# Kernel optimization log

Hardware: AMD Instinct MI355X
Metric: run time of the kernel (lower is better)

Reference implementation:

```python
import jax, jax.numpy as jnp
import numpy as np

NEG = -1e20

def _rope(x):
    # x: (N, L, H, D). Original buffers use inv_freq over D with D/2 entries;
    # sin/cos tiled to full D to broadcast (original code's einsum was under-specified for 4D).
    L, D = x.shape[1], x.shape[3]
    inv_freq = 1.0 / (10000.0 ** (jnp.arange(0, D, 2, dtype=jnp.float32) / D))
    t = jnp.arange(L, dtype=jnp.float32)
    freqs = t[:, None] * inv_freq[None, :]            # (L, D/2)
    sin = jnp.concatenate([jnp.sin(freqs)] * 2, -1)[None, :, None, :]  # (1,L,1,D)
    cos = jnp.concatenate([jnp.cos(freqs)] * 2, -1)[None, :, None, :]
    return x * cos + jnp.flip(x, -1) * sin

def setup_inputs() -> dict:
    key = jax.random.key(0)
    ks = jax.random.split(key, 8)
    N, L, E, H = 2, 1024, 2048, 16
    D = E // H
    s = 0.02
    return {
        "values": jax.random.normal(ks[0], (N, L, E), jnp.float32),
        "keys": jax.random.normal(ks[1], (N, L, E), jnp.float32),
        "queries": jax.random.normal(ks[2], (N, L, E), jnp.float32),
        "mask": jax.random.randint(ks[3], (N, 1, L, L), 0, 2, jnp.int32),
        "Wv": jax.random.normal(ks[4], (D, D), jnp.float32) * s,
        "Wk": jax.random.normal(ks[5], (D, D), jnp.float32) * s,
        "Wq": jax.random.normal(ks[6], (D, D), jnp.float32) * s,
        "Wo": jax.random.normal(ks[7], (E, E), jnp.float32) * s,
        "bo": jnp.zeros((E,), jnp.float32),
    }

def reference(values, keys, queries, mask, Wv, Wk, Wq, Wo, bo):
    N, L, E = queries.shape
    H = 16
    D = E // H
    v = values.reshape(N, L, H, D)
    k = keys.reshape(N, L, H, D)
    q = queries.reshape(N, L, H, D)
    q = _rope(q)
    k = _rope(k)
    # per-head linears (nn.Linear: x @ W.T)
    v = jnp.einsum('nlhd,od->nlho', v, Wv)
    k = jnp.einsum('nlhd,od->nlho', k, Wk)
    q = jnp.einsum('nlhd,od->nlho', q, Wq)
    energy = jnp.einsum('nqhd,nkhd->nhqk', q, k)
    energy = jnp.where(mask == 0, NEG, energy)
    attn = jax.nn.softmax(energy / jnp.sqrt(jnp.float32(E)), axis=3)
    out = jnp.einsum('nhqk,nkhd->nqhd', attn, v).reshape(N, L, E)
    return out @ Wo.T + bo
```

## Files before the change

### kernel.cpp

```cpp
#include <hip/hip_runtime.h>

#define LQ 1024
#define EMB 2048
#define NH 16
#define HD 128
#define RSCALE 0.022097086912079608f

typedef unsigned short u16x8 __attribute__((ext_vector_type(8)));
typedef __bf16 bf16x8 __attribute__((ext_vector_type(8)));
typedef float f32x4 __attribute__((ext_vector_type(4)));
typedef short s16x4 __attribute__((ext_vector_type(4)));

typedef const __attribute__((address_space(1))) unsigned int* gas_t;
typedef __attribute__((address_space(3))) unsigned int* las_t;

__device__ __forceinline__ void glds16(const void* g, void* l){
  __builtin_amdgcn_global_load_lds((gas_t)g, (las_t)l, 16, 0, 0);
}
__device__ __forceinline__ unsigned short f2b(float f){
  unsigned int x = __float_as_uint(f);
  return (unsigned short)((x + 0x7fffu + ((x >> 16) & 1u)) >> 16);
}
__device__ __forceinline__ short f2bs(float f){
  union { __bf16 h; short s; } c; c.h = (__bf16)f; return c.s;
}
__device__ __forceinline__ bf16x8 as_bf(u16x8 u){
  union { u16x8 u; bf16x8 b; } c; c.u = u; return c.b;
}
__device__ __forceinline__ f32x4 mfma16(s16x4 a, s16x4 b, f32x4 c){
  return __builtin_amdgcn_mfma_f32_16x16x16bf16_1k(a, b, c, 0, 0, 0);
}

__global__ __launch_bounds__(256) void k_prep(const float* __restrict__ Wo,
                                              unsigned short* __restrict__ Wob,
                                              const int* __restrict__ M,
                                              unsigned long long* __restrict__ Mb){
  int bx = blockIdx.x, t = threadIdx.x;
  if (bx < 4096) {
    int i = (bx * 256 + t) * 4;
    float4 f = *(const float4*)&Wo[i];
    ushort4 u;
    u.x = f2b(f.x); u.y = f2b(f.y); u.z = f2b(f.z); u.w = f2b(f.w);
    *(ushort4*)&Wob[i] = u;
  } else {
    int w_idx = (bx - 4096) * 4 + (t >> 6);
    int lane = t & 63;
    int n = w_idx >> 14, row = (w_idx >> 4) & 1023, wc = w_idx & 15;
    int v = M[(size_t)n * (LQ * LQ) + (size_t)row * LQ + wc * 64 + lane];
    unsigned long long b = __ballot(v != 0);
    if (lane == 0) Mb[w_idx] = b;
  }
}

__global__ __launch_bounds__(256) void k_proj(
    const float* __restrict__ vals, const float* __restrict__ keys,
    const float* __restrict__ qrys,
    const float* __restrict__ Wv, const float* __restrict__ Wk,
    const float* __restrict__ Wq,
    unsigned short* __restrict__ vp, unsigned short* __restrict__ kp,
    unsigned short* __restrict__ qp)
{
  __shared__ unsigned short Xs[64 * 136];
  __shared__ unsigned short Ws[128 * 136];
  __shared__ float scC[4 * 128], scS[4 * 128];
  int t = threadIdx.x;
  int which = blockIdx.y;
  const float* X; const float* W; unsigned short* OUT; bool rope;
  if (which == 0)      { X = vals; W = Wv; OUT = vp; rope = false; }
  else if (which == 1) { X = keys; W = Wk; OUT = kp; rope = true;  }
  else                 { X = qrys; W = Wq; OUT = qp; rope = true;  }
  float qs = (which == 2) ? RSCALE : 1.0f;
  int m0 = blockIdx.x * 64;

  #pragma unroll
  for (int i = 0; i < 8; ++i) {
    int ci = t + 256 * i;
    int row = ci >> 4, ch = ci & 15;
    float4 a = *(const float4*)&W[row * 128 + ch * 8];
    float4 b = *(const float4*)&W[row * 128 + ch * 8 + 4];
    u16x8 u;
    u[0]=f2b(a.x); u[1]=f2b(a.y); u[2]=f2b(a.z); u[3]=f2b(a.w);
    u[4]=f2b(b.x); u[5]=f2b(b.y); u[6]=f2b(b.z); u[7]=f2b(b.w);
    *(u16x8*)&Ws[row * 136 + ch * 8] = u;
  }
  if (rope) {
    int l0 = (blockIdx.x * 4) & 1023;
    #pragma unroll
    for (int i = 0; i < 2; ++i) {
      int idx = t + 256 * i;
      int li = idx >> 7, d = idx & 127, j = d & 63;
      float inv = 1.0f / powf(10000.0f, (float)(2 * j) * 0.0078125f);
      float ang = (float)(l0 + li) * inv;
      scC[idx] = cosf(ang);
      scS[idx] = sinf(ang);
    }
  }
  __syncthreads();
  #pragma unroll
  for (int i = 0; i < 8; ++i) {
    int fi = t + 256 * i;
    int row = fi >> 5, dq = (fi & 31) * 4;
    int gr = m0 + row;
    float4 x = *(const float4*)&X[(size_t)gr * HD + dq];
    ushort4 u;
    if (rope) {
      int li = row >> 4;
      float4 xm = *(const float4*)&X[(size_t)gr * HD + (124 - dq)];
      float4 c  = *(const float4*)&scC[li * 128 + dq];
      float4 s  = *(const float4*)&scS[li * 128 + dq];
      u.x = f2b(x.x * c.x + xm.w * s.x);
      u.y = f2b(x.y * c.y + xm.z * s.y);
      u.z = f2b(x.z * c.z + xm.y * s.z);
      u.w = f2b(x.w * c.w + xm.x * s.w);
    } else {
      u.x = f2b(x.x); u.y = f2b(x.y); u.z = f2b(x.z); u.w = f2b(x.w);
    }
    *(ushort4*)&Xs[row * 136 + dq] = u;
  }
  __syncthreads();

  int w = t >> 6, lane = t & 63, quad = lane >> 4, n16 = lane & 15;
  f32x4 of[4][2];
  #pragma unroll
  for (int a = 0; a < 4; ++a)
    { of[a][0] = (f32x4){0.f,0.f,0.f,0.f}; of[a][1] = (f32x4){0.f,0.f,0.f,0.f}; }

  #pragma unroll
  for (int kd = 0; kd < 4; ++kd) {
    bf16x8 bfr[2];
    #pragma unroll
    for (int b2 = 0; b2 < 2; ++b2)
      bfr[b2] = as_bf(*(const u16x8*)&Ws[(w * 32 + b2 * 16 + n16) * 136 + kd * 32 + quad * 8]);
    #pragma unroll
    for (int a = 0; a < 4; ++a) {
      bf16x8 af = as_bf(*(const u16x8*)&Xs[(a * 16 + n16) * 136 + kd * 32 + quad * 8]);
      of[a][0] = __builtin_amdgcn_mfma_f32_16x16x32_bf16(af, bfr[0], of[a][0], 0, 0, 0);
      of[a][1] = __builtin_amdgcn_mfma_f32_16x16x32_bf16(af, bfr[1], of[a][1], 0, 0, 0);
    }
  }

  #pragma unroll
  for (int a = 0; a < 4; ++a) {
    #pragma unroll
    for (int b2 = 0; b2 < 2; ++b2) {
      #pragma unroll
      for (int r = 0; r < 4; ++r) {
        int m = m0 + a * 16 + quad * 4 + r;
        int n = m >> 14, l = (m >> 4) & 1023, h = m & 15;
        int o = w * 32 + b2 * 16 + n16;
        OUT[(((size_t)(n * NH + h)) * LQ + l) * HD + o] = f2b(of[a][b2][r] * qs);
      }
    }
  }
}

__global__ __launch_bounds__(256) void k_vtrans(const unsigned short* __restrict__ vp,
                                                unsigned short* __restrict__ vt){
  __shared__ unsigned short Ls[64 * 136];
  int t = threadIdx.x;
  int l0 = blockIdx.x * 64;
  size_t base = (size_t)blockIdx.y * LQ * HD;
  #pragma unroll
  for (int i = 0; i < 4; ++i) {
    int ci = t + 256 * i;
    int row = ci >> 4, ch = ci & 15;
    *(u16x8*)&Ls[row * 136 + ch * 8] =
        *(const u16x8*)&vp[base + (size_t)(l0 + row) * HD + ch * 8];
  }
  __syncthreads();
  #pragma unroll
  for (int i = 0; i < 4; ++i) {
    int idx = t + 256 * i;
    int d = idx & 127, lc = idx >> 7;
    u16x8 pk;
    #pragma unroll
    for (int j = 0; j < 8; ++j) pk[j] = Ls[(lc * 8 + j) * 136 + d];
    *(u16x8*)&vt[base + (size_t)d * LQ + l0 + lc * 8] = pk;
  }
}

__global__ __launch_bounds__(512) void k_attn(
    const unsigned short* __restrict__ qp, const unsigned short* __restrict__ kp,
    const unsigned short* __restrict__ vt, const unsigned long long* __restrict__ Mb,
    unsigned short* __restrict__ ao)
{
  __shared__ unsigned short Ks[2][64 * 128];
  __shared__ unsigned short Vt[2][128 * 64];
  __shared__ float ls[8][16];
  int t = threadIdx.x, w = t >> 6, lane = t & 63, quad = lane >> 4, n16 = lane & 15;
  int grp = w >> 2, wq = w & 3;
  int ub = t & 448;
  int lin = blockIdx.y * gridDim.x + blockIdx.x;
  int xcd = lin & 7, j = lin >> 3;
  int bh = xcd + 8 * (j >> 4);
  int q0 = (j & 15) * 64;
  int nIdx = bh >> 4, h = bh & 15;
  size_t base = (size_t)bh * LQ * HD;
  const unsigned short* Q = qp + base;
  const unsigned short* K = kp + base;
  const unsigned short* V = vt + base;

  bf16x8 qf[4];
  #pragma unroll
  for (int kd = 0; kd < 4; ++kd)
    qf[kd] = as_bf(*(const u16x8*)&Q[(size_t)(q0 + wq * 16 + n16) * HD + kd * 32 + quad * 8]);

  const unsigned long long* MbRow =
      Mb + ((size_t)nIdx * LQ + q0 + wq * 16 + n16) * 16;

  f32x4 of[8];
  #pragma unroll
  for (int c = 0; c < 8; ++c) of[c] = (f32x4){0.f, 0.f, 0.f, 0.f};
  float lp = 0.f;

  for (int p = 0; p < 8; ++p) {
    int k0 = p * 128;
    __syncthreads();
    #pragma unroll
    for (int jj = 0; jj < 2; ++jj) {
      #pragma unroll
      for (int i = 0; i < 2; ++i) {
        int ci = t + 512 * i;
        int krow = ci >> 4, kch = (ci & 15) ^ (krow & 7);
        glds16(&K[(size_t)(k0 + jj * 64 + krow) * HD + kch * 8],
               &Ks[jj][(ub + 512 * i) * 8]);
        int vrow = ci >> 3, vch = (ci & 7) ^ (vrow & 7);
        glds16(&V[(size_t)vrow * LQ + k0 + jj * 64 + vch * 8],
               &Vt[jj][(ub + 512 * i) * 8]);
      }
    }
    unsigned long long mq = MbRow[2 * p + grp];
    __syncthreads();

    unsigned long long msh = mq >> (quad * 4);

    f32x4 sf[4];
    #pragma unroll
    for (int c = 0; c < 4; ++c) sf[c] = (f32x4){0.f, 0.f, 0.f, 0.f};
    __builtin_amdgcn_s_setprio(1);
    #pragma unroll
    for (int kd = 0; kd < 4; ++kd) {
      #pragma unroll
      for (int c = 0; c < 4; ++c) {
        int slot = (kd * 4 + quad) ^ (n16 & 7);
        bf16x8 kv = as_bf(*(const u16x8*)&Ks[grp][(c * 16 + n16) * 128 + slot * 8]);
        sf[c] = __builtin_amdgcn_mfma_f32_16x16x32_bf16(kv, qf[kd], sf[c], 0, 0, 0);
      }
    }
    __builtin_amdgcn_s_setprio(0);
    #pragma unroll
    for (int c = 0; c < 4; ++c) {
      s16x4 pa;
      #pragma unroll
      for (int r = 0; r < 4; ++r) {
        int bit = (int)((msh >> (c * 16 + r)) & 1ull);
        float p = bit ? __expf(sf[c][r]) : 0.f;
        lp += p;
        pa[r] = f2bs(p);
      }
      int cc = 2 * c + (quad >> 1);
      __builtin_amdgcn_s_setprio(1);
      #pragma unroll
      for (int c2 = 0; c2 < 8; ++c2) {
        int row = c2 * 16 + n16;
        int slot = cc ^ (n16 & 7);
        s16x4 vv = *(const s16x4*)&Vt[grp][row * 64 + slot * 8 + (quad & 1) * 4];
        of[c2] = mfma16(pa, vv, of[c2]);
      }
      __builtin_amdgcn_s_setprio(0);
    }
  }

  __syncthreads();
  {
    float s = lp;
    s += __shfl_xor(s, 16);
    s += __shfl_xor(s, 32);
    ls[w][n16] = s;
  }
  float* OF = (float*)&Ks[0][0];
  if (grp == 1) {
    #pragma unroll
    for (int c2 = 0; c2 < 8; ++c2) {
      #pragma unroll
      for (int r = 0; r < 4; ++r) {
        OF[(wq * 16 + quad * 4 + r) * 128 + c2 * 16 + n16] = of[c2][r];
      }
    }
  }
  __syncthreads();
  if (grp == 0) {
    float linv[4];
    #pragma unroll
    for (int r = 0; r < 4; ++r)
      linv[r] = 1.0f / fmaxf(ls[wq][quad * 4 + r] + ls[wq + 4][quad * 4 + r], 1e-30f);
    #pragma unroll
    for (int c2 = 0; c2 < 8; ++c2) {
      #pragma unroll
      for (int r = 0; r < 4; ++r) {
        float v = of[c2][r] + OF[(wq * 16 + quad * 4 + r) * 128 + c2 * 16 + n16];
        ao[((size_t)(nIdx * LQ + q0 + wq * 16 + quad * 4 + r)) * EMB + h * HD + c2 * 16 + n16] =
            f2b(v * linv[r]);
      }
    }
  }
}

__global__ __launch_bounds__(256) void k_outproj(
    const unsigned short* __restrict__ ao, const unsigned short* __restrict__ Wob,
    const float* __restrict__ bo, float* __restrict__ out)
{
  __shared__ unsigned short As[2][128 * 64];
  __shared__ unsigned short Bs[2][64 * 64];
  int t = threadIdx.x;
  int w = t >> 6, lane = t & 63, quad = lane >> 4, n16 = lane & 15;
  int wm = w >> 1, wo = w & 1;
  int m0 = blockIdx.x * 128, o0 = blockIdx.y * 64;
  int ub = (t & 192);

  f32x4 of[4][2];
  #pragma unroll
  for (int a = 0; a < 4; ++a)
    { of[a][0] = (f32x4){0.f,0.f,0.f,0.f}; of[a][1] = (f32x4){0.f,0.f,0.f,0.f}; }

  #pragma unroll
  for (int i = 0; i < 4; ++i) {
    int ci = t + 256 * i;
    int row = ci >> 3, ch = (ci & 7) ^ (row & 7);
    glds16(&ao[(size_t)(m0 + row) * EMB + ch * 8], &As[0][(ub + 256 * i) * 8]);
  }
  #pragma unroll
  for (int i = 0; i < 2; ++i) {
    int ci = t + 256 * i;
    int row = ci >> 3, ch = (ci & 7) ^ (row & 7);
    glds16(&Wob[(size_t)(o0 + row) * EMB + ch * 8], &Bs[0][(ub + 256 * i) * 8]);
  }

  for (int kt = 0; kt < 32; ++kt) {
    int cur = kt & 1;
    __syncthreads();
    if (kt < 31) {
      int k1 = (kt + 1) * 64;
      #pragma unroll
      for (int i = 0; i < 4; ++i) {
        int ci = t + 256 * i;
        int row = ci >> 3, ch = (ci & 7) ^ (row & 7);
        glds16(&ao[(size_t)(m0 + row) * EMB + k1 + ch * 8], &As[1 - cur][(ub + 256 * i) * 8]);
      }
      #pragma unroll
      for (int i = 0; i < 2; ++i) {
        int ci = t + 256 * i;
        int row = ci >> 3, ch = (ci & 7) ^ (row & 7);
        glds16(&Wob[(size_t)(o0 + row) * EMB + k1 + ch * 8], &Bs[1 - cur][(ub + 256 * i) * 8]);
      }
    }
    #pragma unroll
    for (int kd = 0; kd < 2; ++kd) {
      int slot0 = (kd * 4 + quad);
      bf16x8 af[4], bf[2];
      #pragma unroll
      for (int a = 0; a < 4; ++a)
        af[a] = as_bf(*(const u16x8*)&As[cur][(wm * 64 + a * 16 + n16) * 64 + (slot0 ^ (n16 & 7)) * 8]);
      #pragma unroll
      for (int b = 0; b < 2; ++b)
        bf[b] = as_bf(*(const u16x8*)&Bs[cur][(wo * 32 + b * 16 + n16) * 64 + (slot0 ^ (n16 & 7)) * 8]);
      #pragma unroll
      for (int a = 0; a < 4; ++a)
        #pragma unroll
        for (int b = 0; b < 2; ++b)
          of[a][b] = __builtin_amdgcn_mfma_f32_16x16x32_bf16(af[a], bf[b], of[a][b], 0, 0, 0);
    }
  }

  float bb[2] = { bo[o0 + wo * 32 + n16], bo[o0 + wo * 32 + 16 + n16] };
  #pragma unroll
  for (int a = 0; a < 4; ++a) {
    #pragma unroll
    for (int b = 0; b < 2; ++b) {
      #pragma unroll
      for (int r = 0; r < 4; ++r) {
        out[(size_t)(m0 + wm * 64 + a * 16 + quad * 4 + r) * EMB
            + o0 + wo * 32 + b * 16 + n16] = of[a][b][r] + bb[b];
      }
    }
  }
}

extern "C" void kernel_launch(void* const* d_in, const int* in_sizes, int n_in,
                              void* d_out, int out_size, void* d_ws, size_t ws_size,
                              hipStream_t stream) {
  (void)in_sizes; (void)n_in; (void)out_size; (void)ws_size;
  const float* vals = (const float*)d_in[0];
  const float* keys = (const float*)d_in[1];
  const float* qrys = (const float*)d_in[2];
  const int*   mask = (const int*)d_in[3];
  const float* Wv   = (const float*)d_in[4];
  const float* Wk   = (const float*)d_in[5];
  const float* Wq   = (const float*)d_in[6];
  const float* Wo   = (const float*)d_in[7];
  const float* bo   = (const float*)d_in[8];
  float* out = (float*)d_out;

  unsigned short* U  = (unsigned short*)d_ws;
  unsigned short* qp = U;
  unsigned short* kp = U + 4194304;
  unsigned short* vp = U + 8388608;
  unsigned short* vt = U + 12582912;
  unsigned short* ao = U + 16777216;
  unsigned short* Wob= U + 20971520;
  unsigned long long* Mb = (unsigned long long*)(U + 25165824);

  k_prep    <<<dim3(12288),  dim3(256), 0, stream>>>(Wo, Wob, mask, Mb);
  k_proj    <<<dim3(512, 3), dim3(256), 0, stream>>>(vals, keys, qrys, Wv, Wk, Wq,
                                                     vp, kp, qp);
  k_vtrans  <<<dim3(16, 32), dim3(256), 0, stream>>>(vp, vt);
  k_attn    <<<dim3(16, 32), dim3(512), 0, stream>>>(qp, kp, vt, Mb, ao);
  k_outproj <<<dim3(16, 32), dim3(256), 0, stream>>>(ao, Wob, bo, out);
}
```

Before: 207.3 us.

## Pre-swizzle K and V tiles into MFMA fragment order for linear LDS reads

The V transpose kernel now writes V in a per-tile fragment layout that matches exactly what each lane feeds to the PV MFMA. The attention kernel's K loads are also gathered into fragment order during the global-to-LDS copy. This lets the inner loops read LDS with plain lane-contiguous addresses instead of XOR-swizzled ones, aiming to cut address arithmetic and LDS bank conflicts. The cost is scattered global reads for K, since each 16-byte chunk comes from a different row, and a more intricate transpose kernel.

```diff
diff --git a/kernel.cpp b/kernel.cpp
--- a/kernel.cpp
+++ b/kernel.cpp
@@ -155,10 +155,11 @@
 }
 
 __global__ __launch_bounds__(256) void k_vtrans(const unsigned short* __restrict__ vp,
-                                                unsigned short* __restrict__ vt){
+                                                unsigned short* __restrict__ vtF){
   __shared__ unsigned short Ls[64 * 136];
   int t = threadIdx.x;
-  int l0 = blockIdx.x * 64;
+  int kt = blockIdx.x;
+  int l0 = kt * 64;
   size_t base = (size_t)blockIdx.y * LQ * HD;
   #pragma unroll
   for (int i = 0; i < 4; ++i) {
@@ -170,26 +171,32 @@
   __syncthreads();
   #pragma unroll
   for (int i = 0; i < 4; ++i) {
-    int idx = t + 256 * i;
-    int d = idx & 127, lc = idx >> 7;
+    int m = t + 256 * i;
+    int b = m >> 5, w5 = m & 31;
+    int c = b >> 3, c2 = b & 7;
+    int l1 = 2 * w5;
+    int qd = l1 >> 4, nn0 = l1 & 15;
     u16x8 pk;
     #pragma unroll
-    for (int j = 0; j < 8; ++j) pk[j] = Ls[(lc * 8 + j) * 136 + d];
-    *(u16x8*)&vt[base + (size_t)d * LQ + l0 + lc * 8] = pk;
+    for (int j = 0; j < 4; ++j)
+      pk[j] = Ls[(c * 16 + qd * 4 + j) * 136 + c2 * 16 + nn0];
+    #pragma unroll
+    for (int j = 0; j < 4; ++j)
+      pk[4 + j] = Ls[(c * 16 + qd * 4 + j) * 136 + c2 * 16 + nn0 + 1];
+    *(u16x8*)&vtF[base + (size_t)kt * 8192 + (size_t)m * 8] = pk;
   }
 }
 
 __global__ __launch_bounds__(512) void k_attn(
     const unsigned short* __restrict__ qp, const unsigned short* __restrict__ kp,
-    const unsigned short* __restrict__ vt, const unsigned long long* __restrict__ Mb,
+    const unsigned short* __restrict__ vtF, const unsigned long long* __restrict__ Mb,
     unsigned short* __restrict__ ao)
 {
-  __shared__ unsigned short Ks[2][64 * 128];
-  __shared__ unsigned short Vt[2][128 * 64];
+  __shared__ unsigned short KsF[2][8192];
+  __shared__ unsigned short VsF[2][8192];
   __shared__ float ls[8][16];
   int t = threadIdx.x, w = t >> 6, lane = t & 63, quad = lane >> 4, n16 = lane & 15;
   int grp = w >> 2, wq = w & 3;
-  int ub = t & 448;
   int lin = blockIdx.y * gridDim.x + blockIdx.x;
   int xcd = lin & 7, j = lin >> 3;
   int bh = xcd + 8 * (j >> 4);
@@ -198,7 +205,7 @@
   size_t base = (size_t)bh * LQ * HD;
   const unsigned short* Q = qp + base;
   const unsigned short* K = kp + base;
-  const unsigned short* V = vt + base;
+  const unsigned short* VF = vtF + base;
 
   bf16x8 qf[4];
   #pragma unroll
@@ -218,15 +225,15 @@
     __syncthreads();
     #pragma unroll
     for (int jj = 0; jj < 2; ++jj) {
+      int kt = 2 * p + jj;
       #pragma unroll
       for (int i = 0; i < 2; ++i) {
-        int ci = t + 512 * i;
-        int krow = ci >> 4, kch = (ci & 15) ^ (krow & 7);
-        glds16(&K[(size_t)(k0 + jj * 64 + krow) * HD + kch * 8],
-               &Ks[jj][(ub + 512 * i) * 8]);
-        int vrow = ci >> 3, vch = (ci & 7) ^ (vrow & 7);
-        glds16(&V[(size_t)vrow * LQ + k0 + jj * 64 + vch * 8],
-               &Vt[jj][(ub + 512 * i) * 8]);
+        int D = t + 512 * i;
+        int nn = D & 15, qq = (D >> 4) & 3, cc = (D >> 6) & 3, kd = D >> 8;
+        glds16(&K[(size_t)(k0 + jj * 64 + cc * 16 + nn) * HD + (kd * 4 + qq) * 8],
+               &KsF[jj][(size_t)D * 8]);
+        glds16(&VF[(size_t)kt * 8192 + (size_t)D * 8],
+               &VsF[jj][(size_t)D * 8]);
       }
     }
     unsigned long long mq = MbRow[2 * p + grp];
@@ -242,8 +249,7 @@
     for (int kd = 0; kd < 4; ++kd) {
       #pragma unroll
       for (int c = 0; c < 4; ++c) {
-        int slot = (kd * 4 + quad) ^ (n16 & 7);
-        bf16x8 kv = as_bf(*(const u16x8*)&Ks[grp][(c * 16 + n16) * 128 + slot * 8]);
+        bf16x8 kv = as_bf(*(const u16x8*)&KsF[grp][((kd * 4 + c) * 64 + lane) * 8]);
         sf[c] = __builtin_amdgcn_mfma_f32_16x16x32_bf16(kv, qf[kd], sf[c], 0, 0, 0);
       }
     }
@@ -258,13 +264,10 @@
         lp += p;
         pa[r] = f2bs(p);
       }
-      int cc = 2 * c + (quad >> 1);
       __builtin_amdgcn_s_setprio(1);
       #pragma unroll
       for (int c2 = 0; c2 < 8; ++c2) {
-        int row = c2 * 16 + n16;
-        int slot = cc ^ (n16 & 7);
-        s16x4 vv = *(const s16x4*)&Vt[grp][row * 64 + slot * 8 + (quad & 1) * 4];
+        s16x4 vv = *(const s16x4*)&VsF[grp][((c * 8 + c2) * 64 + lane) * 4];
         of[c2] = mfma16(pa, vv, of[c2]);
       }
       __builtin_amdgcn_s_setprio(0);
@@ -278,7 +281,7 @@
     s += __shfl_xor(s, 32);
     ls[w][n16] = s;
   }
-  float* OF = (float*)&Ks[0][0];
+  float* OF = (float*)&KsF[0][0];
   if (grp == 1) {
     #pragma unroll
     for (int c2 = 0; c2 < 8; ++c2) {
@@ -405,7 +408,7 @@
   unsigned short* qp = U;
   unsigned short* kp = U + 4194304;
   unsigned short* vp = U + 8388608;
-  unsigned short* vt = U + 12582912;
+  unsigned short* vtF= U + 12582912;
   unsigned short* ao = U + 16777216;
   unsigned short* Wob= U + 20971520;
   unsigned long long* Mb = (unsigned long long*)(U + 25165824);
@@ -413,7 +416,7 @@
   k_prep    <<<dim3(12288),  dim3(256), 0, stream>>>(Wo, Wob, mask, Mb);
   k_proj    <<<dim3(512, 3), dim3(256), 0, stream>>>(vals, keys, qrys, Wv, Wk, Wq,
                                                      vp, kp, qp);
-  k_vtrans  <<<dim3(16, 32), dim3(256), 0, stream>>>(vp, vt);
-  k_attn    <<<dim3(16, 32), dim3(512), 0, stream>>>(qp, kp, vt, Mb, ao);
+  k_vtrans  <<<dim3(16, 32), dim3(256), 0, stream>>>(vp, vtF);
+  k_attn    <<<dim3(16, 32), dim3(512), 0, stream>>>(qp, kp, vtF, Mb, ao);
   k_outproj <<<dim3(16, 32), dim3(256), 0, stream>>>(ao, Wob, bo, out);
 }
```

Result: no change. 206.2 us (-0.5%).
